# Performance work log

Hardware: AMD Instinct MI355X
Metric: run time of the kernel (lower is better)

## Reference

```python
import jax, jax.numpy as jnp
import numpy as np

N = 100000
E = 600000
F_IN = 128
HID = 256
C = 64


def setup_inputs() -> dict:
    key = jax.random.key(0)
    ks = jax.random.split(key, 6)
    x = jax.random.normal(ks[0], (N, F_IN), dtype=jnp.float32)
    edge_index = jax.random.randint(ks[1], (2, E), 0, N, dtype=jnp.int64)
    W1 = jax.random.normal(ks[2], (F_IN, HID), dtype=jnp.float32) * (1.0 / np.sqrt(F_IN))
    b1 = jnp.zeros((HID,), dtype=jnp.float32)
    W2 = jax.random.normal(ks[3], (HID, C), dtype=jnp.float32) * (1.0 / np.sqrt(HID))
    b2 = jnp.zeros((C,), dtype=jnp.float32)
    return {"x": x, "W1": W1, "b1": b1, "W2": W2, "b2": b2, "edge_index": edge_index}


def _gcn_conv(h, W, b, src, dst, norm, self_w):
    # h: [N, F_in] -> [N, F_out]; symmetric-normalized aggregation over A+I
    h = h @ W  # [N, F_out]
    agg = jax.ops.segment_sum(h[src] * norm[:, None], dst, num_segments=N)
    agg = agg + h * self_w[:, None]  # self-loop contribution d^{-1/2}*d^{-1/2}
    return agg + b


def reference(x, W1, b1, W2, b2, edge_index):
    src, dst = edge_index[0], edge_index[1]
    # degree of A + I (self-loops added): 1 + in-degree
    deg = jnp.ones((N,), dtype=x.dtype).at[dst].add(1.0)
    dinv = jax.lax.rsqrt(deg)
    norm = dinv[src] * dinv[dst]  # [E]
    self_w = dinv * dinv          # [N]

    h = _gcn_conv(x, W1, b1, src, dst, norm, self_w)
    h = jax.nn.relu(h)
    # dropout is identity in eval mode (training=False)
    out = _gcn_conv(h, W2, b2, src, dst, norm, self_w)
    return jax.nn.log_softmax(out, axis=1)
```

## Files before the change

kernel.cpp:

```cpp
#include <hip/hip_runtime.h>
#include <cstdint>
#include <cstddef>

#define N_NODES 100000
#define N_EDGES 600000
#define F_IN    128
#define HID     256
#define NC      64
#define NB_SCAN 391

typedef __attribute__((ext_vector_type(8))) short bf16x8;
typedef __attribute__((ext_vector_type(4))) float f32x4;

__device__ __forceinline__ unsigned short f2bf(float f) {
    unsigned int u = __float_as_uint(f);
    u = (u + 0x7FFFu + ((u >> 16) & 1u)) >> 16;
    return (unsigned short)u;
}
__device__ __forceinline__ float bf2f(unsigned short u) {
    return __uint_as_float(((unsigned int)u) << 16);
}

__global__ void k_detect(const int* __restrict__ ei_words, int* __restrict__ mode) {
    if (blockIdx.x == 0 && threadIdx.x == 0) {
        int allz = 1;
        for (int i = 0; i < 64; ++i) {
            long long s = (long long)i * (N_EDGES - 1) / 63;
            if (ei_words[2 * s + 1] != 0) { allz = 0; break; }
        }
        *mode = allz;
    }
}

__device__ __forceinline__ int load_idx(const void* ei, int m, long long i) {
    return m ? (int)((const long long*)ei)[i] : ((const int*)ei)[i];
}

__global__ void k_zero(int* __restrict__ p, int n) {
    int i = blockIdx.x * blockDim.x + threadIdx.x;
    if (i < n) p[i] = 0;
}

__global__ void k_hist(const void* __restrict__ ei, const int* __restrict__ mode,
                       int* __restrict__ deg) {
    int e = blockIdx.x * blockDim.x + threadIdx.x;
    if (e >= N_EDGES) return;
    int d = load_idx(ei, *mode, (long long)N_EDGES + e);
    atomicAdd(&deg[d], 1);
}

__global__ void k_scanA(const int* __restrict__ deg, int* __restrict__ ptmp,
                        int* __restrict__ bsum) {
    __shared__ int sm[256];
    int i = blockIdx.x * 256 + threadIdx.x;
    int v = (i < N_NODES) ? deg[i] : 0;
    sm[threadIdx.x] = v;
    __syncthreads();
    for (int off = 1; off < 256; off <<= 1) {
        int t = (threadIdx.x >= off) ? sm[threadIdx.x - off] : 0;
        __syncthreads();
        sm[threadIdx.x] += t;
        __syncthreads();
    }
    if (i < N_NODES) ptmp[i] = sm[threadIdx.x] - v;
    if (threadIdx.x == 255) bsum[blockIdx.x] = sm[255];
}

__global__ void k_scanB(int* __restrict__ bsum) {
    __shared__ int sm[512];
    int i = threadIdx.x;
    int v = (i < NB_SCAN) ? bsum[i] : 0;
    sm[i] = v;
    __syncthreads();
    for (int off = 1; off < 512; off <<= 1) {
        int t = (i >= off) ? sm[i - off] : 0;
        __syncthreads();
        sm[i] += t;
        __syncthreads();
    }
    if (i < NB_SCAN) bsum[i] = sm[i] - v;
}

__global__ void k_scanC(const int* __restrict__ deg, const int* __restrict__ ptmp,
                        const int* __restrict__ bsum, int* __restrict__ row_ptr,
                        int* __restrict__ cursor, float* __restrict__ dinv) {
    int i = blockIdx.x * 256 + threadIdx.x;
    if (i < N_NODES) {
        int rp = ptmp[i] + bsum[blockIdx.x];
        row_ptr[i] = rp;
        cursor[i]  = rp;
        dinv[i]    = rsqrtf(1.0f + (float)deg[i]);
    }
    if (i == 0) row_ptr[N_NODES] = N_EDGES;
}

__global__ void k_fill(const void* __restrict__ ei, const int* __restrict__ mode,
                       int* __restrict__ cursor, int* __restrict__ csr_src) {
    int e = blockIdx.x * blockDim.x + threadIdx.x;
    if (e >= N_EDGES) return;
    int m = *mode;
    int s = load_idx(ei, m, e);
    int d = load_idx(ei, m, (long long)N_EDGES + e);
    int pos = atomicAdd(&cursor[d], 1);
    csr_src[pos] = s;
}

__global__ void k_w1t(const float* __restrict__ W1, unsigned short* __restrict__ W1T) {
    int i = blockIdx.x * 256 + threadIdx.x;
    int k = i >> 8, n = i & 255;
    W1T[n * F_IN + k] = f2bf(W1[i]);
}
__global__ void k_w2t(const float* __restrict__ W2, unsigned short* __restrict__ W2T) {
    int i = blockIdx.x * 256 + threadIdx.x;
    int k = i >> 6, n = i & 63;
    W2T[n * HID + k] = f2bf(W2[i]);
}

__global__ void k_xbf(const float* __restrict__ x, unsigned short* __restrict__ xbf) {
    int i = blockIdx.x * 256 + threadIdx.x;
    const float4* xr = (const float4*)x;
    float4 a = xr[(size_t)i * 2];
    float4 b = xr[(size_t)i * 2 + 1];
    bf16x8 o;
    o[0] = (short)f2bf(a.x); o[1] = (short)f2bf(a.y);
    o[2] = (short)f2bf(a.z); o[3] = (short)f2bf(a.w);
    o[4] = (short)f2bf(b.x); o[5] = (short)f2bf(b.y);
    o[6] = (short)f2bf(b.z); o[7] = (short)f2bf(b.w);
    *(bf16x8*)(xbf + (size_t)i * 8) = o;
}

__global__ void k_gather1(const unsigned short* __restrict__ xbf,
                          const int* __restrict__ row_ptr,
                          const int* __restrict__ csr_src, const float* __restrict__ dinv,
                          unsigned short* __restrict__ px) {
    int g = threadIdx.x >> 4;
    int j = threadIdx.x & 15;
    int n = blockIdx.x * 16 + g;
    float dn = dinv[n];
    bf16x8 sv = *(const bf16x8*)(xbf + (size_t)n * F_IN + j * 8);
    float acc[8];
#pragma unroll
    for (int t = 0; t < 8; ++t) acc[t] = bf2f((unsigned short)sv[t]) * dn;
    int e0 = row_ptr[n], e1 = row_ptr[n + 1];
    for (int k = e0; k < e1; ++k) {
        int s = csr_src[k];
        float w = dinv[s];
        bf16x8 v = *(const bf16x8*)(xbf + (size_t)s * F_IN + j * 8);
#pragma unroll
        for (int t = 0; t < 8; ++t)
            acc[t] = fmaf(bf2f((unsigned short)v[t]), w, acc[t]);
    }
    bf16x8 o;
#pragma unroll
    for (int t = 0; t < 8; ++t) o[t] = (short)f2bf(acc[t] * dn);
    *(bf16x8*)(px + (size_t)n * F_IN + j * 8) = o;
}

__global__ __launch_bounds__(256) void k_mlp_fused(
        const unsigned short* __restrict__ px, const unsigned short* __restrict__ W1T,
        const float* __restrict__ b1, const unsigned short* __restrict__ W2T,
        unsigned short* __restrict__ hx2) {
    __shared__ unsigned short hlds[64 * HID];
    const int lane = threadIdx.x & 63;
    const int w    = threadIdx.x >> 6;
    const int l15  = lane & 15, lhi = lane >> 4;
    const int row0 = blockIdx.x * 64;

    {
        const int col0 = w * 64;
        f32x4 acc[4][4];
#pragma unroll
        for (int mt = 0; mt < 4; ++mt)
#pragma unroll
            for (int nt = 0; nt < 4; ++nt) acc[mt][nt] = (f32x4){0.f, 0.f, 0.f, 0.f};

#pragma unroll
        for (int ks = 0; ks < 4; ++ks) {
            bf16x8 a[4];
#pragma unroll
            for (int mt = 0; mt < 4; ++mt)
                a[mt] = *(const bf16x8*)(px + (size_t)(row0 + mt * 16 + l15) * F_IN + ks * 32 + lhi * 8);
#pragma unroll
            for (int nt = 0; nt < 4; ++nt) {
                bf16x8 b = *(const bf16x8*)(W1T + (size_t)(col0 + nt * 16 + l15) * F_IN + ks * 32 + lhi * 8);
#pragma unroll
                for (int mt = 0; mt < 4; ++mt)
                    acc[mt][nt] = __builtin_amdgcn_mfma_f32_16x16x32_bf16(b, a[mt], acc[mt][nt], 0, 0, 0);
            }
        }

#pragma unroll
        for (int mt = 0; mt < 4; ++mt) {
            const int lr = mt * 16 + l15;
#pragma unroll
            for (int nt = 0; nt < 4; ++nt) {
                int c0 = col0 + nt * 16 + lhi * 4;
                float4 bb = *(const float4*)(b1 + c0);
                ushort4 o;
                o.x = f2bf(fmaxf(acc[mt][nt][0] + bb.x, 0.f));
                o.y = f2bf(fmaxf(acc[mt][nt][1] + bb.y, 0.f));
                o.z = f2bf(fmaxf(acc[mt][nt][2] + bb.z, 0.f));
                o.w = f2bf(fmaxf(acc[mt][nt][3] + bb.w, 0.f));
                unsigned byte = (unsigned)(lr * (HID * 2) + c0 * 2) ^ ((lr & 7) << 4);
                *(ushort4*)((char*)hlds + byte) = o;
            }
        }
    }
    __syncthreads();

    {
        const int lr = w * 16 + l15;
        bf16x8 a2[8];
#pragma unroll
        for (int ks = 0; ks < 8; ++ks) {
            unsigned byte = (unsigned)(lr * (HID * 2) + ks * 64 + lhi * 16) ^ ((lr & 7) << 4);
            a2[ks] = *(const bf16x8*)((const char*)hlds + byte);
        }
        f32x4 acc2[4];
#pragma unroll
        for (int nt = 0; nt < 4; ++nt) acc2[nt] = (f32x4){0.f, 0.f, 0.f, 0.f};
#pragma unroll
        for (int nt = 0; nt < 4; ++nt) {
            const unsigned short* pb = W2T + (size_t)(nt * 16 + l15) * HID + lhi * 8;
#pragma unroll
            for (int ks = 0; ks < 8; ++ks) {
                bf16x8 b = *(const bf16x8*)(pb + ks * 32);
                acc2[nt] = __builtin_amdgcn_mfma_f32_16x16x32_bf16(b, a2[ks], acc2[nt], 0, 0, 0);
            }
        }
        const int r = row0 + lr;
        if (r < N_NODES) {
#pragma unroll
            for (int nt = 0; nt < 4; ++nt) {
                int c0 = nt * 16 + lhi * 4;
                ushort4 o;
                o.x = f2bf(acc2[nt][0]); o.y = f2bf(acc2[nt][1]);
                o.z = f2bf(acc2[nt][2]); o.w = f2bf(acc2[nt][3]);
                *(ushort4*)(hx2 + (size_t)r * NC + c0) = o;
            }
        }
    }
}

__global__ void k_gather2sm(const unsigned short* __restrict__ hx2,
                            const int* __restrict__ row_ptr,
                            const int* __restrict__ csr_src, const float* __restrict__ dinv,
                            const float* __restrict__ b2, float* __restrict__ out) {
    int g = threadIdx.x >> 4;
    int j = threadIdx.x & 15;
    int n = blockIdx.x * 16 + g;
    float dn = dinv[n];
    ushort4 sv = *(const ushort4*)(hx2 + (size_t)n * NC + j * 4);
    float ax = bf2f(sv.x) * dn, ay = bf2f(sv.y) * dn,
          az = bf2f(sv.z) * dn, aw = bf2f(sv.w) * dn;
    int e0 = row_ptr[n], e1 = row_ptr[n + 1];
    for (int k = e0; k < e1; ++k) {
        int s = csr_src[k];
        float wv = dinv[s];
        ushort4 v = *(const ushort4*)(hx2 + (size_t)s * NC + j * 4);
        ax = fmaf(bf2f(v.x), wv, ax); ay = fmaf(bf2f(v.y), wv, ay);
        az = fmaf(bf2f(v.z), wv, az); aw = fmaf(bf2f(v.w), wv, aw);
    }
    const float4 b = ((const float4*)b2)[j];
    float4 o;
    o.x = fmaf(ax, dn, b.x); o.y = fmaf(ay, dn, b.y);
    o.z = fmaf(az, dn, b.z); o.w = fmaf(aw, dn, b.w);
    float mx = fmaxf(fmaxf(o.x, o.y), fmaxf(o.z, o.w));
#pragma unroll
    for (int msk = 8; msk; msk >>= 1) mx = fmaxf(mx, __shfl_xor(mx, msk));
    float s4 = expf(o.x - mx) + expf(o.y - mx) + expf(o.z - mx) + expf(o.w - mx);
#pragma unroll
    for (int msk = 8; msk; msk >>= 1) s4 += __shfl_xor(s4, msk);
    float ls = mx + logf(s4);
    o.x -= ls; o.y -= ls; o.z -= ls; o.w -= ls;
    ((float4*)out)[(size_t)n * 16 + j] = o;
}

extern "C" void kernel_launch(void* const* d_in, const int* in_sizes, int n_in,
                              void* d_out, int out_size, void* d_ws, size_t ws_size,
                              hipStream_t stream) {
    const float* x  = (const float*)d_in[0];
    const float* W1 = (const float*)d_in[1];
    const float* b1 = (const float*)d_in[2];
    const float* W2 = (const float*)d_in[3];
    const float* b2 = (const float*)d_in[4];
    const void*  ei = d_in[5];
    float* out = (float*)d_out;

    char* ws = (char*)d_ws;
    size_t off = 0;
    auto alloc = [&](size_t bytes) {
        char* p = ws + off;
        off += (bytes + 255) & ~(size_t)255;
        return p;
    };
    int*            mode    = (int*)            alloc(4);
    int*            deg     = (int*)            alloc((size_t)N_NODES * 4);
    int*            ptmp    = (int*)            alloc((size_t)N_NODES * 4);
    int*            bsum    = (int*)            alloc(4096);
    int*            row_ptr = (int*)            alloc((size_t)(N_NODES + 1) * 4);
    int*            cursor  = (int*)            alloc((size_t)N_NODES * 4);
    float*          dinv    = (float*)          alloc((size_t)N_NODES * 4);
    int*            csr_src = (int*)            alloc((size_t)N_EDGES * 4);
    unsigned short* W1T     = (unsigned short*) alloc((size_t)F_IN * HID * 2);
    unsigned short* W2T     = (unsigned short*) alloc((size_t)HID * NC * 2);
    unsigned short* xbf     = (unsigned short*) alloc((size_t)N_NODES * F_IN * 2);
    unsigned short* px      = (unsigned short*) alloc((size_t)(N_NODES + 64) * F_IN * 2);
    unsigned short* hx2     = (unsigned short*) alloc((size_t)(N_NODES + 64) * NC * 2);

    k_detect<<<1, 64, 0, stream>>>((const int*)ei, mode);

    k_zero<<<(N_NODES + 255) / 256, 256, 0, stream>>>(deg, N_NODES);
    k_hist<<<(N_EDGES + 255) / 256, 256, 0, stream>>>(ei, mode, deg);
    k_scanA<<<NB_SCAN, 256, 0, stream>>>(deg, ptmp, bsum);
    k_scanB<<<1, 512, 0, stream>>>(bsum);
    k_scanC<<<NB_SCAN, 256, 0, stream>>>(deg, ptmp, bsum, row_ptr, cursor, dinv);
    k_fill<<<(N_EDGES + 255) / 256, 256, 0, stream>>>(ei, mode, cursor, csr_src);

    k_w1t<<<F_IN * HID / 256, 256, 0, stream>>>(W1, W1T);
    k_w2t<<<HID * NC / 256, 256, 0, stream>>>(W2, W2T);
    k_xbf<<<N_NODES * F_IN / 8 / 256, 256, 0, stream>>>(x, xbf);

    k_gather1<<<N_NODES / 16, 256, 0, stream>>>(xbf, row_ptr, csr_src, dinv, px);
    k_mlp_fused<<<(N_NODES + 63) / 64, 256, 0, stream>>>(px, W1T, b1, W2T, hx2);
    k_gather2sm<<<N_NODES / 16, 256, 0, stream>>>(hx2, row_ptr, csr_src, dinv, b2, out);
}
```

Baseline: 220.1 us.

## Merge conversion kernels into one launch and halve MLP row tile

Merges the three small conversion kernels (x to bf16, W1 and W2 transpose) into one launch, with each block picking its job by block index. This saves two kernel launches. The fused MLP kernel now processes 32 rows per block instead of 64. It uses half the LDS, fewer accumulators, a launch-bounds hint for 4 blocks per CU, and a second-layer split where each wave computes 16 rows by 32 columns. This is meant to raise occupancy and spread work over more blocks, at the cost of reloading W1T and W2T per block twice as often.

After: 221.2 us. About the same (+0.5%).

```diff
diff --git a/kernel.cpp b/kernel.cpp
--- a/kernel.cpp
+++ b/kernel.cpp
@@ -105,28 +105,34 @@
     csr_src[pos] = s;
 }
 
-__global__ void k_w1t(const float* __restrict__ W1, unsigned short* __restrict__ W1T) {
-    int i = blockIdx.x * 256 + threadIdx.x;
-    int k = i >> 8, n = i & 255;
-    W1T[n * F_IN + k] = f2bf(W1[i]);
-}
-__global__ void k_w2t(const float* __restrict__ W2, unsigned short* __restrict__ W2T) {
-    int i = blockIdx.x * 256 + threadIdx.x;
-    int k = i >> 6, n = i & 63;
-    W2T[n * HID + k] = f2bf(W2[i]);
-}
-
-__global__ void k_xbf(const float* __restrict__ x, unsigned short* __restrict__ xbf) {
-    int i = blockIdx.x * 256 + threadIdx.x;
-    const float4* xr = (const float4*)x;
-    float4 a = xr[(size_t)i * 2];
-    float4 b = xr[(size_t)i * 2 + 1];
-    bf16x8 o;
-    o[0] = (short)f2bf(a.x); o[1] = (short)f2bf(a.y);
-    o[2] = (short)f2bf(a.z); o[3] = (short)f2bf(a.w);
-    o[4] = (short)f2bf(b.x); o[5] = (short)f2bf(b.y);
-    o[6] = (short)f2bf(b.z); o[7] = (short)f2bf(b.w);
-    *(bf16x8*)(xbf + (size_t)i * 8) = o;
+#define XB_BLOCKS (N_NODES * F_IN / 8 / 256)
+#define W1_BLOCKS (F_IN * HID / 256)
+#define W2_BLOCKS (HID * NC / 256)
+__global__ void k_prep(const float* __restrict__ x, const float* __restrict__ W1,
+                       const float* __restrict__ W2, unsigned short* __restrict__ xbf,
+                       unsigned short* __restrict__ W1T, unsigned short* __restrict__ W2T) {
+    int bid = blockIdx.x;
+    int tid = threadIdx.x;
+    if (bid < XB_BLOCKS) {
+        int i = bid * 256 + tid;
+        const float4* xr = (const float4*)x;
+        float4 a = xr[(size_t)i * 2];
+        float4 b = xr[(size_t)i * 2 + 1];
+        bf16x8 o;
+        o[0] = (short)f2bf(a.x); o[1] = (short)f2bf(a.y);
+        o[2] = (short)f2bf(a.z); o[3] = (short)f2bf(a.w);
+        o[4] = (short)f2bf(b.x); o[5] = (short)f2bf(b.y);
+        o[6] = (short)f2bf(b.z); o[7] = (short)f2bf(b.w);
+        *(bf16x8*)(xbf + (size_t)i * 8) = o;
+    } else if (bid < XB_BLOCKS + W1_BLOCKS) {
+        int i = (bid - XB_BLOCKS) * 256 + tid;
+        int k = i >> 8, n = i & 255;
+        W1T[n * F_IN + k] = f2bf(W1[i]);
+    } else {
+        int i = (bid - XB_BLOCKS - W1_BLOCKS) * 256 + tid;
+        int k = i >> 6, n = i & 63;
+        W2T[n * HID + k] = f2bf(W2[i]);
+    }
 }
 
 __global__ void k_gather1(const unsigned short* __restrict__ xbf,
@@ -156,41 +162,44 @@
     *(bf16x8*)(px + (size_t)n * F_IN + j * 8) = o;
 }
 
-__global__ __launch_bounds__(256) void k_mlp_fused(
+__global__ __launch_bounds__(256, 4) void k_mlp_fused(
         const unsigned short* __restrict__ px, const unsigned short* __restrict__ W1T,
         const float* __restrict__ b1, const unsigned short* __restrict__ W2T,
         unsigned short* __restrict__ hx2) {
-    __shared__ unsigned short hlds[64 * HID];
+    __shared__ unsigned short hlds[32 * HID];
     const int lane = threadIdx.x & 63;
     const int w    = threadIdx.x >> 6;
     const int l15  = lane & 15, lhi = lane >> 4;
-    const int row0 = blockIdx.x * 64;
+    const int row0 = blockIdx.x * 32;
 
     {
         const int col0 = w * 64;
-        f32x4 acc[4][4];
-#pragma unroll
-        for (int mt = 0; mt < 4; ++mt)
+        bf16x8 a[4][2];
+#pragma unroll
+        for (int ks = 0; ks < 4; ++ks)
+#pragma unroll
+            for (int mt = 0; mt < 2; ++mt)
+                a[ks][mt] = *(const bf16x8*)(px + (size_t)(row0 + mt * 16 + l15) * F_IN + ks * 32 + lhi * 8);
+
+        f32x4 acc[2][4];
+#pragma unroll
+        for (int mt = 0; mt < 2; ++mt)
 #pragma unroll
             for (int nt = 0; nt < 4; ++nt) acc[mt][nt] = (f32x4){0.f, 0.f, 0.f, 0.f};
 
 #pragma unroll
         for (int ks = 0; ks < 4; ++ks) {
-            bf16x8 a[4];
-#pragma unroll
-            for (int mt = 0; mt < 4; ++mt)
-                a[mt] = *(const bf16x8*)(px + (size_t)(row0 + mt * 16 + l15) * F_IN + ks * 32 + lhi * 8);
 #pragma unroll
             for (int nt = 0; nt < 4; ++nt) {
                 bf16x8 b = *(const bf16x8*)(W1T + (size_t)(col0 + nt * 16 + l15) * F_IN + ks * 32 + lhi * 8);
 #pragma unroll
-                for (int mt = 0; mt < 4; ++mt)
-                    acc[mt][nt] = __builtin_amdgcn_mfma_f32_16x16x32_bf16(b, a[mt], acc[mt][nt], 0, 0, 0);
+                for (int mt = 0; mt < 2; ++mt)
+                    acc[mt][nt] = __builtin_amdgcn_mfma_f32_16x16x32_bf16(b, a[ks][mt], acc[mt][nt], 0, 0, 0);
             }
         }
 
 #pragma unroll
-        for (int mt = 0; mt < 4; ++mt) {
+        for (int mt = 0; mt < 2; ++mt) {
             const int lr = mt * 16 + l15;
 #pragma unroll
             for (int nt = 0; nt < 4; ++nt) {
@@ -209,19 +218,20 @@
     __syncthreads();
 
     {
-        const int lr = w * 16 + l15;
+        const int lr = (w & 1) * 16 + l15;
+        const int cb = (w >> 1) * 32;
         bf16x8 a2[8];
 #pragma unroll
         for (int ks = 0; ks < 8; ++ks) {
             unsigned byte = (unsigned)(lr * (HID * 2) + ks * 64 + lhi * 16) ^ ((lr & 7) << 4);
             a2[ks] = *(const bf16x8*)((const char*)hlds + byte);
         }
-        f32x4 acc2[4];
-#pragma unroll
-        for (int nt = 0; nt < 4; ++nt) acc2[nt] = (f32x4){0.f, 0.f, 0.f, 0.f};
-#pragma unroll
-        for (int nt = 0; nt < 4; ++nt) {
-            const unsigned short* pb = W2T + (size_t)(nt * 16 + l15) * HID + lhi * 8;
+        f32x4 acc2[2];
+#pragma unroll
+        for (int nt = 0; nt < 2; ++nt) acc2[nt] = (f32x4){0.f, 0.f, 0.f, 0.f};
+#pragma unroll
+        for (int nt = 0; nt < 2; ++nt) {
+            const unsigned short* pb = W2T + (size_t)(cb + nt * 16 + l15) * HID + lhi * 8;
 #pragma unroll
             for (int ks = 0; ks < 8; ++ks) {
                 bf16x8 b = *(const bf16x8*)(pb + ks * 32);
@@ -229,15 +239,13 @@
             }
         }
         const int r = row0 + lr;
-        if (r < N_NODES) {
-#pragma unroll
-            for (int nt = 0; nt < 4; ++nt) {
-                int c0 = nt * 16 + lhi * 4;
-                ushort4 o;
-                o.x = f2bf(acc2[nt][0]); o.y = f2bf(acc2[nt][1]);
-                o.z = f2bf(acc2[nt][2]); o.w = f2bf(acc2[nt][3]);
-                *(ushort4*)(hx2 + (size_t)r * NC + c0) = o;
-            }
+#pragma unroll
+        for (int nt = 0; nt < 2; ++nt) {
+            int c0 = cb + nt * 16 + lhi * 4;
+            ushort4 o;
+            o.x = f2bf(acc2[nt][0]); o.y = f2bf(acc2[nt][1]);
+            o.z = f2bf(acc2[nt][2]); o.w = f2bf(acc2[nt][3]);
+            *(ushort4*)(hx2 + (size_t)r * NC + c0) = o;
         }
     }
 }
@@ -317,11 +325,9 @@
     k_scanC<<<NB_SCAN, 256, 0, stream>>>(deg, ptmp, bsum, row_ptr, cursor, dinv);
     k_fill<<<(N_EDGES + 255) / 256, 256, 0, stream>>>(ei, mode, cursor, csr_src);
 
-    k_w1t<<<F_IN * HID / 256, 256, 0, stream>>>(W1, W1T);
-    k_w2t<<<HID * NC / 256, 256, 0, stream>>>(W2, W2T);
-    k_xbf<<<N_NODES * F_IN / 8 / 256, 256, 0, stream>>>(x, xbf);
+    k_prep<<<XB_BLOCKS + W1_BLOCKS + W2_BLOCKS, 256, 0, stream>>>(x, W1, W2, xbf, W1T, W2T);
 
     k_gather1<<<N_NODES / 16, 256, 0, stream>>>(xbf, row_ptr, csr_src, dinv, px);
-    k_mlp_fused<<<(N_NODES + 63) / 64, 256, 0, stream>>>(px, W1T, b1, W2T, hx2);
+    k_mlp_fused<<<N_NODES / 32, 256, 0, stream>>>(px, W1T, b1, W2T, hx2);
     k_gather2sm<<<N_NODES / 16, 256, 0, stream>>>(hx2, row_ptr, csr_src, dinv, b2, out);
 }
```
